# Kernel optimization log

Measured on AMD Instinct MI355X. Metric: run time of the kernel, lower is better.

## Reference

```python
import jax, jax.numpy as jnp
import numpy as np

N_TAPS = 2
N_DELAY = 1
N_ITER = 3
EPS_MODEL = 1e-5   # LaplaceModel clamp eps (eps_models['laplace'])
EPS = 1e-3         # ISS divide/clamp eps


def mag_sq(x):
    return jnp.real(x) ** 2 + jnp.imag(x) ** 2


def laplace_weights(X):
    # Laplace source model: w[..., c, n] = 1 / (2 * ||X[..., c, :, n]||_2), broadcast over freq
    # X: (..., c, f, n) complex -> weights: (..., c, 1, n) real
    denom = 2.0 * jnp.sqrt(jnp.sum(mag_sq(X), axis=-2, keepdims=True))
    return 1.0 / jnp.maximum(denom, EPS_MODEL)


def iss_type1(src, Xc, weights):
    # Equation (9): update vector for source `src`
    Xs = Xc[..., src, :, :]  # (..., f, n)
    v_num = jnp.mean(weights * Xc * jnp.conj(Xs)[..., None, :, :], axis=-1)  # (..., c, f)
    v_denom = jnp.mean(weights * mag_sq(Xs)[..., None, :, :], axis=-1)       # (..., c, f) real
    v = v_num / jnp.maximum(v_denom, EPS)
    v_s = 1.0 - 1.0 / jnp.sqrt(jnp.maximum(v_denom[..., src, :], EPS))
    v = v.at[..., src, :].set(v_s.astype(v.dtype))
    return v


def iss_type2(src, tap, Xc, X_bar, weights):
    # update vector for dereverberation tap (src, tap)
    Xst = X_bar[..., src, :, tap, :]  # (..., f, n)
    v_num = jnp.mean(weights * Xc * jnp.conj(Xst)[..., None, :, :], axis=-1)
    # NOTE: the source code does NOT apply the 1/n_frames norm to v_denom here
    v_denom = jnp.sum(weights * mag_sq(Xst)[..., None, :, :], axis=-1)
    return v_num / jnp.maximum(v_denom, EPS)


def epoch_update(Xloc, Xc, W, X_bar, n_chan):
    weights = laplace_weights(Xloc)  # (..., c, 1, n)
    g = jnp.maximum(jnp.mean(mag_sq(Xloc), axis=(-2, -1), keepdims=True), 1e-5)
    Xloc = Xloc / jnp.sqrt(g)
    weights = weights * g
    for src in range(n_chan):
        v = iss_type1(src, Xc, weights)  # (..., c, f)
        Xc = Xc - v[..., None] * Xc[..., src, :, :][..., None, :, :]
        W = W - v[..., None] * W[..., src, :, :][..., None, :, :]
    for src in range(n_chan):
        for tap in range(N_TAPS):
            v = iss_type2(src, tap, Xc, X_bar, weights)
            Xc = Xc - v[..., None] * X_bar[..., src, :, tap, :][..., None, :, :]
    return Xloc, Xc, W


def auxiva_t_iss(X):
    batch = X.shape[:-3]
    n_chan, n_freq, n_frames = X.shape[-3:]
    T, D = N_TAPS, N_DELAY
    # hankel view of left-padded signal; keep only the T oldest rows (delayed taps)
    X_pad = jnp.pad(X, [(0, 0)] * (X.ndim - 1) + [(T + D, 0)])
    # X_bar: (..., c, f, T, n), X_bar[..., tap, t] = X[..., t - (T + D) + tap]
    X_bar = jnp.stack([X_pad[..., t:t + n_frames] for t in range(T)], axis=-2)
    eye = jnp.eye(n_chan, dtype=X.dtype)
    W = jnp.broadcast_to(eye[:, None, :], batch + (n_chan, n_freq, n_chan))
    Xloc = X  # the (buggy-but-faithful) local X that only gets renormalized each epoch
    Xc = X    # self.X, the demixed signal updated by ISS
    for _ in range(N_ITER):
        Xloc, Xc, W = epoch_update(Xloc, Xc, W, X_bar, n_chan)
    # projection back: a_f = (W_f^T)^{-1} e1 per frequency
    WT = jnp.swapaxes(jnp.swapaxes(W, -3, -2), -2, -1)  # (..., f, c, c)
    e1 = jnp.zeros((n_chan, 1), dtype=X.dtype).at[0, 0].set(1.0)
    a = jnp.linalg.solve(WT, e1)       # (..., f, c, 1)
    a = jnp.swapaxes(a, -3, -2)        # (..., c, f, 1)
    return Xc * a


def setup_inputs() -> dict:
    key = jax.random.key(0)
    k1, k2 = jax.random.split(key)
    shape = (4, 4, 257, 1024)  # (batch, n_chan, n_freq, n_frames)
    X_real = jax.random.normal(k1, shape, dtype=jnp.float32)
    X_imag = jax.random.normal(k2, shape, dtype=jnp.float32)
    return {"X_real": X_real, "X_imag": X_imag}


def reference(X_real, X_imag):
    X = jax.lax.complex(X_real, X_imag)
    return auxiva_t_iss(X)
```

## Files before the change

kernel.cpp:

```cpp
#include <hip/hip_runtime.h>
#include <math.h>

#define NB 4
#define NC 4
#define NF 257
#define NFR 1024
#define NTOT (NB * NC * NF * NFR)
#define NBC (NB * NC)
#define EPSV 1e-3f
#define EPS_MODEL 1e-5f
#define NCHUNK 8

typedef float v2f __attribute__((ext_vector_type(2)));

__device__ float g_Spart[NCHUNK * NBC * NFR];

__device__ __forceinline__ float dpp_red_sum(float v) {
  v += __int_as_float(__builtin_amdgcn_update_dpp(0, __float_as_int(v), 0x111, 0xf, 0xf, true));
  v += __int_as_float(__builtin_amdgcn_update_dpp(0, __float_as_int(v), 0x112, 0xf, 0xf, true));
  v += __int_as_float(__builtin_amdgcn_update_dpp(0, __float_as_int(v), 0x114, 0xf, 0xf, true));
  v += __int_as_float(__builtin_amdgcn_update_dpp(0, __float_as_int(v), 0x118, 0xf, 0xf, true));
  v += __int_as_float(__builtin_amdgcn_update_dpp(0, __float_as_int(v), 0x142, 0xa, 0xf, true));
  v += __int_as_float(__builtin_amdgcn_update_dpp(0, __float_as_int(v), 0x143, 0xc, 0xf, true));
  return v;
}

__global__ __launch_bounds__(256) void k_colsum(const float* __restrict__ Xr,
                                                const float* __restrict__ Xi) {
  const int bc = blockIdx.x;
  const int fc = blockIdx.y;
  const int q = threadIdx.x;
  int f0 = fc * 33;
  int f1 = f0 + 33; if (f1 > NF) f1 = NF;
  float4 s = make_float4(0.f, 0.f, 0.f, 0.f);
  for (int f = f0; f < f1; ++f) {
    float4 a = reinterpret_cast<const float4*>(Xr + (bc * NF + f) * NFR)[q];
    float4 b = reinterpret_cast<const float4*>(Xi + (bc * NF + f) * NFR)[q];
    s.x += a.x * a.x + b.x * b.x;
    s.y += a.y * a.y + b.y * b.y;
    s.z += a.z * a.z + b.z * b.z;
    s.w += a.w * a.w + b.w * b.w;
  }
  reinterpret_cast<float4*>(g_Spart + (fc * NBC + bc) * NFR)[q] = s;
}

__device__ __forceinline__ void block_reduce12(float* __restrict__ p,
                                               float (*red)[2][12], int buf,
                                               int lane, int wvid,
                                               float* __restrict__ s) {
#pragma unroll
  for (int k = 0; k < 12; ++k) p[k] = dpp_red_sum(p[k]);
  if (lane == 63) {
    float4* dst = reinterpret_cast<float4*>(&red[buf][wvid][0]);
    dst[0] = make_float4(p[0], p[1], p[2], p[3]);
    dst[1] = make_float4(p[4], p[5], p[6], p[7]);
    dst[2] = make_float4(p[8], p[9], p[10], p[11]);
  }
  __syncthreads();
  const float4* r = reinterpret_cast<const float4*>(&red[buf][0][0]);
#pragma unroll
  for (int k = 0; k < 3; ++k) {
    float4 a = r[k], b = r[3 + k];
    s[4 * k + 0] = a.x + b.x;
    s[4 * k + 1] = a.y + b.y;
    s[4 * k + 2] = a.z + b.z;
    s[4 * k + 3] = a.w + b.w;
  }
}

__device__ __forceinline__ void block_reduce4(float* p, float (*red)[2][12],
                                              int buf, int lane, int wvid) {
#pragma unroll
  for (int k = 0; k < 4; ++k) p[k] = dpp_red_sum(p[k]);
  if (lane == 63) {
    float4* dst = reinterpret_cast<float4*>(&red[buf][wvid][0]);
    dst[0] = make_float4(p[0], p[1], p[2], p[3]);
  }
  __syncthreads();
  const float4* r = reinterpret_cast<const float4*>(&red[buf][0][0]);
  float4 a = r[0], b = r[3];
  p[0] = a.x + b.x;
  p[1] = a.y + b.y;
  p[2] = a.z + b.z;
  p[3] = a.w + b.w;
}

template <int SRC>
__device__ __forceinline__ void t1_sweep(v2f (&xcr)[NC][4], v2f (&xci)[NC][4],
                                         v2f (&w2)[NC][4],
                                         float (&Wre)[NC][NC], float (&Wim)[NC][NC],
                                         float (*red)[2][12], int& buf,
                                         int lane, int wvid, int tid, float invN) {
  v2f p2[12];
#pragma unroll
  for (int k = 0; k < 12; ++k) p2[k] = (v2f){0.f, 0.f};
#pragma unroll
  for (int h = 0; h < 4; ++h) {
    v2f xsr = xcr[SRC][h], xsi = xci[SRC][h];
    v2f msq = xsr * xsr + xsi * xsi;
#pragma unroll
    for (int c = 0; c < NC; ++c) {
      v2f wv = w2[c][h];
      if (c != SRC) {
        const int q = (c < SRC) ? c : c - 1;
        p2[q]     += wv * (xcr[c][h] * xsr + xci[c][h] * xsi);
        p2[3 + q] += wv * (xci[c][h] * xsr - xcr[c][h] * xsi);
      }
      p2[6 + c] += wv * msq;
    }
  }
  float p[12];
#pragma unroll
  for (int k = 0; k < 12; ++k) p[k] = p2[k].x + p2[k].y;
  float s12[12];
  block_reduce12(p, red, buf, lane, wvid, s12);
  buf ^= 1;

  float vr[NC], vi[NC];
#pragma unroll
  for (int c = 0; c < NC; ++c) {
    float den = fmaxf(s12[6 + c] * invN, EPSV);
    if (c == SRC) {
      vr[c] = 1.f - __builtin_amdgcn_rsqf(den);
      vi[c] = 0.f;
    } else {
      const int q = (c < SRC) ? c : c - 1;
      float sc = invN * __builtin_amdgcn_rcpf(den);
      vr[c] = s12[q] * sc;
      vi[c] = s12[3 + q] * sc;
    }
  }
#pragma unroll
  for (int h = 0; h < 4; ++h) {
    v2f xsr = xcr[SRC][h], xsi = xci[SRC][h];
#pragma unroll
    for (int c = 0; c < NC; ++c) {
      xcr[c][h] -= xsr * vr[c] - xsi * vi[c];
      xci[c][h] -= xsi * vr[c] + xsr * vi[c];
    }
  }
  if (tid < 16) {
    int c = tid >> 2, j = tid & 3;
    float wsr = Wre[SRC][j], wsi = Wim[SRC][j];
    float wcr = Wre[c][j],   wci = Wim[c][j];
    float vrc = (c == 0) ? vr[0] : (c == 1) ? vr[1] : (c == 2) ? vr[2] : vr[3];
    float vic = (c == 0) ? vi[0] : (c == 1) ? vi[1] : (c == 2) ? vi[2] : vi[3];
    Wre[c][j] = wcr - (vrc * wsr - vic * wsi);
    Wim[c][j] = wci - (vrc * wsi + vic * wsr);
  }
}

__global__ __launch_bounds__(128, 2) void k_main(const float* __restrict__ Xr,
                                                 const float* __restrict__ Xi,
                                                 float* __restrict__ out, int nout) {
  const int blk = blockIdx.x;
  const int b = blk / NF, f = blk % NF;
  const int tid = threadIdx.x;
  const int lane = tid & 63, wvid = tid >> 6;
  const float invN = 1.f / (float)NFR;

  __shared__ float Sown[NC][NFR];
  __shared__ float red[2][2][12];
  __shared__ float Wre[NC][NC], Wim[NC][NC];
  __shared__ float abc[8];

  v2f xcr[NC][4], xci[NC][4];
  int rowbase[NC];
#pragma unroll
  for (int c = 0; c < NC; ++c) {
    rowbase[c] = ((b * NC + c) * NF + f) * NFR;
    const float4* pr = reinterpret_cast<const float4*>(Xr + rowbase[c]);
    const float4* pi = reinterpret_cast<const float4*>(Xi + rowbase[c]);
    float4 a0 = pr[2 * tid], a1 = pr[2 * tid + 1];
    float4 b0 = pi[2 * tid], b1 = pi[2 * tid + 1];
    xcr[c][0] = (v2f){a0.x, a0.y}; xcr[c][1] = (v2f){a0.z, a0.w};
    xcr[c][2] = (v2f){a1.x, a1.y}; xcr[c][3] = (v2f){a1.z, a1.w};
    xci[c][0] = (v2f){b0.x, b0.y}; xci[c][1] = (v2f){b0.z, b0.w};
    xci[c][2] = (v2f){b1.x, b1.y}; xci[c][3] = (v2f){b1.z, b1.w};
  }
  if (tid < 16) {
    Wre[tid >> 2][tid & 3] = ((tid >> 2) == (tid & 3)) ? 1.f : 0.f;
    Wim[tid >> 2][tid & 3] = 0.f;
  }

  int buf = 0;

  float s0v[4];
  {
    float acc[NC][8];
#pragma unroll
    for (int c = 0; c < NC; ++c)
#pragma unroll
      for (int j = 0; j < 8; ++j) acc[c][j] = 0.f;
#pragma unroll 1
    for (int fc = 0; fc < NCHUNK; ++fc) {
#pragma unroll
      for (int c = 0; c < NC; ++c) {
        const float4* pp =
            reinterpret_cast<const float4*>(g_Spart + (fc * NBC + b * NC + c) * NFR);
        float4 a0 = pp[2 * tid], a1 = pp[2 * tid + 1];
        acc[c][0] += a0.x; acc[c][1] += a0.y; acc[c][2] += a0.z; acc[c][3] += a0.w;
        acc[c][4] += a1.x; acc[c][5] += a1.y; acc[c][6] += a1.z; acc[c][7] += a1.w;
      }
    }
    float p4[4];
#pragma unroll
    for (int c = 0; c < NC; ++c) {
#pragma unroll
      for (int j = 0; j < 8; ++j) Sown[c][8 * tid + j] = acc[c][j];
      p4[c] = ((acc[c][0] + acc[c][1]) + (acc[c][2] + acc[c][3])) +
              ((acc[c][4] + acc[c][5]) + (acc[c][6] + acc[c][7]));
    }
    block_reduce4(p4, red, buf, lane, wvid);
    buf ^= 1;
#pragma unroll
    for (int c = 0; c < NC; ++c) s0v[c] = p4[c] / (float)(NF * NFR);
  }
  float Prun[4] = {1.f, 1.f, 1.f, 1.f};

  v2f w2[NC][4];

  for (int e = 0; e < 3; ++e) {
#pragma unroll
    for (int c = 0; c < NC; ++c) {
      float g = fmaxf(s0v[c] / Prun[c], 1e-5f);
      float sc = __builtin_amdgcn_rcpf(Prun[c]);
      Prun[c] *= g;
      float wv[8];
#pragma unroll
      for (int j = 0; j < 8; ++j) {
        float sv = Sown[c][8 * tid + j];
        wv[j] = g * __builtin_amdgcn_rcpf(fmaxf(2.f * __builtin_amdgcn_sqrtf(sv * sc), EPS_MODEL));
      }
#pragma unroll
      for (int h = 0; h < 4; ++h) w2[c][h] = (v2f){wv[2 * h], wv[2 * h + 1]};
    }

    t1_sweep<0>(xcr, xci, w2, Wre, Wim, red, buf, lane, wvid, tid, invN);
    t1_sweep<1>(xcr, xci, w2, Wre, Wim, red, buf, lane, wvid, tid, invN);
    t1_sweep<2>(xcr, xci, w2, Wre, Wim, red, buf, lane, wvid, tid, invN);
    t1_sweep<3>(xcr, xci, w2, Wre, Wim, red, buf, lane, wvid, tid, invN);

#pragma unroll 1
    for (int src = 0; src < NC; ++src) {
      const float4* pr = reinterpret_cast<const float4*>(Xr + rowbase[src]);
      const float4* pi = reinterpret_cast<const float4*>(Xi + rowbase[src]);
      float4 A4r = make_float4(0.f, 0.f, 0.f, 0.f), A4i = A4r;
      if (tid > 0) { A4r = pr[2 * tid - 1]; A4i = pi[2 * tid - 1]; }
      float4 B4r = pr[2 * tid], B4i = pi[2 * tid];
      float4 C4r = pr[2 * tid + 1], C4i = pi[2 * tid + 1];
      float wr[9] = {A4r.y, A4r.z, A4r.w, B4r.x, B4r.y, B4r.z, B4r.w, C4r.x, C4r.y};
      float wi[9] = {A4i.y, A4i.z, A4i.w, B4i.x, B4i.y, B4i.z, B4i.w, C4i.x, C4i.y};
#pragma unroll
      for (int tap = 0; tap < 2; ++tap) {
        v2f xs_r[4], xs_i[4];
#pragma unroll
        for (int h = 0; h < 4; ++h) {
          xs_r[h] = (v2f){wr[tap + 2 * h], wr[tap + 2 * h + 1]};
          xs_i[h] = (v2f){wi[tap + 2 * h], wi[tap + 2 * h + 1]};
        }
        v2f p2[12];
#pragma unroll
        for (int k = 0; k < 12; ++k) p2[k] = (v2f){0.f, 0.f};
#pragma unroll
        for (int h = 0; h < 4; ++h) {
          v2f xsr = xs_r[h], xsi = xs_i[h];
          v2f msq = xsr * xsr + xsi * xsi;
#pragma unroll
          for (int c = 0; c < NC; ++c) {
            v2f wv = w2[c][h];
            p2[c]     += wv * (xcr[c][h] * xsr + xci[c][h] * xsi);
            p2[4 + c] += wv * (xci[c][h] * xsr - xcr[c][h] * xsi);
            p2[8 + c] += wv * msq;
          }
        }
        float p[12];
#pragma unroll
        for (int k = 0; k < 12; ++k) p[k] = p2[k].x + p2[k].y;
        float s12[12];
        block_reduce12(p, red, buf, lane, wvid, s12);
        buf ^= 1;

        float vr[NC], vi[NC];
#pragma unroll
        for (int c = 0; c < NC; ++c) {
          float den = fmaxf(s12[8 + c], EPSV);
          float sc = invN * __builtin_amdgcn_rcpf(den);
          vr[c] = s12[c] * sc;
          vi[c] = s12[4 + c] * sc;
        }
#pragma unroll
        for (int h = 0; h < 4; ++h) {
          v2f xsr = xs_r[h], xsi = xs_i[h];
#pragma unroll
          for (int c = 0; c < NC; ++c) {
            xcr[c][h] -= xsr * vr[c] - xsi * vi[c];
            xci[c][h] -= xsi * vr[c] + xsr * vi[c];
          }
        }
      }
    }
  }

  __syncthreads();
  if (tid == 0) {
    float Ar[4][4], Ai[4][4];
    float br[4] = {1.f, 0.f, 0.f, 0.f}, bi[4] = {0.f, 0.f, 0.f, 0.f};
#pragma unroll
    for (int i = 0; i < 4; ++i)
#pragma unroll
      for (int j = 0; j < 4; ++j) {
        Ar[i][j] = Wre[j][i];
        Ai[i][j] = Wim[j][i];
      }
    for (int k = 0; k < 4; ++k) {
      int piv = k;
      float best = Ar[k][k] * Ar[k][k] + Ai[k][k] * Ai[k][k];
      for (int i = k + 1; i < 4; ++i) {
        float m = Ar[i][k] * Ar[i][k] + Ai[i][k] * Ai[i][k];
        if (m > best) { best = m; piv = i; }
      }
      if (piv != k) {
        for (int j = 0; j < 4; ++j) {
          float t = Ar[k][j]; Ar[k][j] = Ar[piv][j]; Ar[piv][j] = t;
          t = Ai[k][j]; Ai[k][j] = Ai[piv][j]; Ai[piv][j] = t;
        }
        float t = br[k]; br[k] = br[piv]; br[piv] = t;
        t = bi[k]; bi[k] = bi[piv]; bi[piv] = t;
      }
      float dr = Ar[k][k], di = Ai[k][k];
      float inv = 1.f / (dr * dr + di * di);
      for (int i = k + 1; i < 4; ++i) {
        float fr = (Ar[i][k] * dr + Ai[i][k] * di) * inv;
        float fi = (Ai[i][k] * dr - Ar[i][k] * di) * inv;
        for (int j = k; j < 4; ++j) {
          Ar[i][j] -= fr * Ar[k][j] - fi * Ai[k][j];
          Ai[i][j] -= fr * Ai[k][j] + fi * Ar[k][j];
        }
        br[i] -= fr * br[k] - fi * bi[k];
        bi[i] -= fr * bi[k] + fi * br[k];
      }
    }
    float ar[4], ai[4];
    for (int k = 3; k >= 0; --k) {
      float sr = br[k], si = bi[k];
      for (int j = k + 1; j < 4; ++j) {
        sr -= Ar[k][j] * ar[j] - Ai[k][j] * ai[j];
        si -= Ar[k][j] * ai[j] + Ai[k][j] * ar[j];
      }
      float dr = Ar[k][k], di = Ai[k][k];
      float inv = 1.f / (dr * dr + di * di);
      ar[k] = (sr * dr + si * di) * inv;
      ai[k] = (si * dr - sr * di) * inv;
    }
#pragma unroll
    for (int c = 0; c < 4; ++c) { abc[c] = ar[c]; abc[4 + c] = ai[c]; }
  }
  __syncthreads();

#pragma unroll
  for (int c = 0; c < NC; ++c) {
    float ar = abc[c], ai2 = abc[4 + c];
    if (rowbase[c] + 8 * tid + 7 < nout) {
      float4* po = reinterpret_cast<float4*>(out + rowbase[c]);
      v2f o0 = xcr[c][0] * ar - xci[c][0] * ai2;
      v2f o1 = xcr[c][1] * ar - xci[c][1] * ai2;
      v2f o2 = xcr[c][2] * ar - xci[c][2] * ai2;
      v2f o3 = xcr[c][3] * ar - xci[c][3] * ai2;
      po[2 * tid]     = make_float4(o0.x, o0.y, o1.x, o1.y);
      po[2 * tid + 1] = make_float4(o2.x, o2.y, o3.x, o3.y);
    }
  }
}

extern "C" void kernel_launch(void* const* d_in, const int* in_sizes, int n_in,
                              void* d_out, int out_size, void* d_ws, size_t ws_size,
                              hipStream_t stream) {
  const float* Xr = (const float*)d_in[0];
  const float* Xi = (const float*)d_in[1];
  float* out = (float*)d_out;

  dim3 g1(16, NCHUNK);
  k_colsum<<<g1, 256, 0, stream>>>(Xr, Xi);
  k_main<<<NB * NF, 128, 0, stream>>>(Xr, Xi, out, out_size);
}
```

Baseline: 196.5 us.

## Prefetch next source's X_bar rows, transpose Sown layout, relax occupancy bound

The global loads of the lagged source rows used by the type-2 dereverberation sweep are now software-prefetched one source ahead, including across epochs, so their latency overlaps the current source's compute. Sown shared memory is transposed to [c][j][tid], so each per-thread access is strided by one word across threads, which avoids LDS bank conflicts. The launch-bounds minimum-blocks hint drops from 2 to 1, giving the compiler more registers for the extra prefetch buffers at the risk of lower occupancy.

```diff
diff --git a/kernel.cpp b/kernel.cpp
--- a/kernel.cpp
+++ b/kernel.cpp
@@ -150,7 +150,7 @@
   }
 }
 
-__global__ __launch_bounds__(128, 2) void k_main(const float* __restrict__ Xr,
+__global__ __launch_bounds__(128, 1) void k_main(const float* __restrict__ Xr,
                                                  const float* __restrict__ Xi,
                                                  float* __restrict__ out, int nout) {
   const int blk = blockIdx.x;
@@ -159,7 +159,7 @@
   const int lane = tid & 63, wvid = tid >> 6;
   const float invN = 1.f / (float)NFR;
 
-  __shared__ float Sown[NC][NFR];
+  __shared__ float Sown[NC][8][128];
   __shared__ float red[2][2][12];
   __shared__ float Wre[NC][NC], Wim[NC][NC];
   __shared__ float abc[8];
@@ -207,7 +207,7 @@
 #pragma unroll
     for (int c = 0; c < NC; ++c) {
 #pragma unroll
-      for (int j = 0; j < 8; ++j) Sown[c][8 * tid + j] = acc[c][j];
+      for (int j = 0; j < 8; ++j) Sown[c][j][tid] = acc[c][j];
       p4[c] = ((acc[c][0] + acc[c][1]) + (acc[c][2] + acc[c][3])) +
               ((acc[c][4] + acc[c][5]) + (acc[c][6] + acc[c][7]));
     }
@@ -219,6 +219,16 @@
   float Prun[4] = {1.f, 1.f, 1.f, 1.f};
 
   v2f w2[NC][4];
+
+  float4 nA4r, nA4i, nB4r, nB4i, nC4r, nC4i;
+  {
+    const float4* pr0 = reinterpret_cast<const float4*>(Xr + rowbase[0]);
+    const float4* pi0 = reinterpret_cast<const float4*>(Xi + rowbase[0]);
+    nA4r = make_float4(0.f, 0.f, 0.f, 0.f); nA4i = nA4r;
+    if (tid > 0) { nA4r = pr0[2 * tid - 1]; nA4i = pi0[2 * tid - 1]; }
+    nB4r = pr0[2 * tid];     nB4i = pi0[2 * tid];
+    nC4r = pr0[2 * tid + 1]; nC4i = pi0[2 * tid + 1];
+  }
 
   for (int e = 0; e < 3; ++e) {
 #pragma unroll
@@ -229,7 +239,7 @@
       float wv[8];
 #pragma unroll
       for (int j = 0; j < 8; ++j) {
-        float sv = Sown[c][8 * tid + j];
+        float sv = Sown[c][j][tid];
         wv[j] = g * __builtin_amdgcn_rcpf(fmaxf(2.f * __builtin_amdgcn_sqrtf(sv * sc), EPS_MODEL));
       }
 #pragma unroll
@@ -243,14 +253,17 @@
 
 #pragma unroll 1
     for (int src = 0; src < NC; ++src) {
-      const float4* pr = reinterpret_cast<const float4*>(Xr + rowbase[src]);
-      const float4* pi = reinterpret_cast<const float4*>(Xi + rowbase[src]);
-      float4 A4r = make_float4(0.f, 0.f, 0.f, 0.f), A4i = A4r;
-      if (tid > 0) { A4r = pr[2 * tid - 1]; A4i = pi[2 * tid - 1]; }
-      float4 B4r = pr[2 * tid], B4i = pi[2 * tid];
-      float4 C4r = pr[2 * tid + 1], C4i = pi[2 * tid + 1];
-      float wr[9] = {A4r.y, A4r.z, A4r.w, B4r.x, B4r.y, B4r.z, B4r.w, C4r.x, C4r.y};
-      float wi[9] = {A4i.y, A4i.z, A4i.w, B4i.x, B4i.y, B4i.z, B4i.w, C4i.x, C4i.y};
+      float wr[9] = {nA4r.y, nA4r.z, nA4r.w, nB4r.x, nB4r.y, nB4r.z, nB4r.w, nC4r.x, nC4r.y};
+      float wi[9] = {nA4i.y, nA4i.z, nA4i.w, nB4i.x, nB4i.y, nB4i.z, nB4i.w, nC4i.x, nC4i.y};
+      {
+        const int nsrc = (src + 1) & 3;
+        const float4* prn = reinterpret_cast<const float4*>(Xr + rowbase[nsrc]);
+        const float4* pin = reinterpret_cast<const float4*>(Xi + rowbase[nsrc]);
+        nA4r = make_float4(0.f, 0.f, 0.f, 0.f); nA4i = nA4r;
+        if (tid > 0) { nA4r = prn[2 * tid - 1]; nA4i = pin[2 * tid - 1]; }
+        nB4r = prn[2 * tid];     nB4i = pin[2 * tid];
+        nC4r = prn[2 * tid + 1]; nC4i = pin[2 * tid + 1];
+      }
 #pragma unroll
       for (int tap = 0; tap < 2; ++tap) {
         v2f xs_r[4], xs_i[4];
```

Result: no change. 196.1 us (-0.2%).
